# Kernel tuning notes

Measured on AMD Instinct MI355X. Metric: run time of the kernel, lower is better.

Reference implementation:

```python
import jax, jax.numpy as jnp
import numpy as np

H, DH = 16, 64  # heads, dim_head; inner = H*DH = 1024
EPS = 1e-5


def _ln(t, g, b):
    mu = jnp.mean(t, axis=-1, keepdims=True)
    var = jnp.var(t, axis=-1, keepdims=True)
    return (t - mu) * jax.lax.rsqrt(var + EPS) * g + b


def _split_heads(t):
    b, n, _ = t.shape
    return t.reshape(b, n, H, DH).transpose(0, 2, 1, 3)  # (b,h,n,dh)


def setup_inputs() -> dict:
    key = jax.random.key(0)
    ks = jax.random.split(key, 5)
    B, S, M, D = 16, 64, 4096, 1024  # S must equal DH (see source einsum quirk)
    return {
        "x": jax.random.normal(ks[0], (B, S, D), jnp.float32),
        "latents": jax.random.normal(ks[1], (B, M, D), jnp.float32),
        "ln_x_g": jnp.ones((D,), jnp.float32),
        "ln_x_b": jnp.zeros((D,), jnp.float32),
        "ln_l_g": jnp.ones((D,), jnp.float32),
        "ln_l_b": jnp.zeros((D,), jnp.float32),
        "Wq": jax.random.normal(ks[2], (D, H * DH), jnp.float32) * 0.02,
        "Wkv": jax.random.normal(ks[3], (D, 2 * H * DH), jnp.float32) * 0.02,
        "Wout": jax.random.normal(ks[4], (H * DH, D), jnp.float32) * 0.02,
    }


def reference(x, latents, ln_x_g, ln_x_b, ln_l_g, ln_l_b, Wq, Wkv, Wout):
    scale = DH ** -0.5
    xn = _ln(x, ln_x_g, ln_x_b)          # (B,S,D)
    ln = _ln(latents, ln_l_g, ln_l_b)    # (B,M,D)
    q = _split_heads(ln @ Wq) * scale    # (B,H,M,DH)
    k, v = map(_split_heads, jnp.split(xn @ Wkv, 2, axis=-1))  # (B,H,S,DH)
    sim = jnp.einsum('bhid,bhjd->bhij', q, k)                  # (B,H,M,S)
    sim = sim - jax.lax.stop_gradient(jnp.max(sim, axis=-1, keepdims=True))
    attn = jax.nn.softmax(sim, axis=-1)
    # Faithful to source: einsum('b h i d, b h j d -> b h i j', attn, v)
    # contracts attn's S dim with v's DH dim (requires S == DH); out = attn @ v^T.
    out = jnp.einsum('bhis,bhjs->bhij', attn, v)               # (B,H,M,S)
    b, _, m, _ = out.shape
    out = out.transpose(0, 2, 1, 3).reshape(b, m, H * DH)      # (B,M,inner)
    return out @ Wout                                          # (B,M,D)
```

## Files before the change

kernel.cpp:

```cpp
#include <hip/hip_runtime.h>
#include <stdint.h>

#define B_ 16
#define S_ 64
#define M_ 4096
#define D_ 1024
#define H_ 16
#define DH_ 64

typedef unsigned short ushort_t;
typedef __attribute__((ext_vector_type(8))) __bf16 bfrag;
typedef __attribute__((ext_vector_type(4))) float f32x4;

__device__ __forceinline__ ushort_t f2bf(float f) {
  union { float f; uint32_t u; } v; v.f = f;
  uint32_t r = v.u + 0x7fffu + ((v.u >> 16) & 1u);
  return (ushort_t)(r >> 16);
}

__device__ __forceinline__ void gload_lds16(const void* g, void* l) {
  __builtin_amdgcn_global_load_lds((const __attribute__((address_space(1))) void*)g,
                                   (__attribute__((address_space(3))) void*)l, 16, 0, 0);
}

__device__ __forceinline__ f32x4 mfma16x16x32(bfrag a, bfrag b, f32x4 c) {
  return __builtin_amdgcn_mfma_f32_16x16x32_bf16(a, b, c, 0, 0, 0);
}

__device__ __forceinline__ int fsw(int r) { return (((r >> 2) & 3) << 1) | (r & 1); }

__global__ __launch_bounds__(256) void ln_rows_kernel(
    const float* __restrict__ x, const float* __restrict__ g,
    const float* __restrict__ bta, ushort_t* __restrict__ out) {
  const int row = blockIdx.x;
  const int t = threadIdx.x;
  const float4* xr = (const float4*)(x + (size_t)row * D_);
  float4 v = xr[t];
  float s = v.x + v.y + v.z + v.w;
  float ss = v.x * v.x + v.y * v.y + v.z * v.z + v.w * v.w;
#pragma unroll
  for (int o = 32; o >= 1; o >>= 1) { s += __shfl_down(s, o); ss += __shfl_down(ss, o); }
  __shared__ float red[16];
  const int wid = t >> 6;
  if ((t & 63) == 0) { red[wid] = s; red[8 + wid] = ss; }
  __syncthreads();
  float tot = red[0] + red[1] + red[2] + red[3];
  float tot2 = red[8] + red[9] + red[10] + red[11];
  float mu = tot * (1.0f / D_);
  float var = tot2 * (1.0f / D_) - mu * mu;
  float rstd = rsqrtf(var + 1e-5f);
  float4 gg = ((const float4*)g)[t];
  float4 bb = ((const float4*)bta)[t];
  ushort_t ob[4];
  ob[0] = f2bf((v.x - mu) * rstd * gg.x + bb.x);
  ob[1] = f2bf((v.y - mu) * rstd * gg.y + bb.y);
  ob[2] = f2bf((v.z - mu) * rstd * gg.z + bb.z);
  ob[3] = f2bf((v.w - mu) * rstd * gg.w + bb.w);
  *(uint2*)(out + (size_t)row * D_ + t * 4) = *(const uint2*)ob;
}

__global__ void transpose_cast_kernel(const float* __restrict__ W, ushort_t* __restrict__ WT,
                                      int N, float scale) {
  __shared__ float tile[32][33];
  const int n0 = blockIdx.x * 32, k0 = blockIdx.y * 32;
  const int tx = threadIdx.x, ty = threadIdx.y;
#pragma unroll
  for (int i = ty; i < 32; i += 8)
    tile[i][tx] = W[(size_t)(k0 + i) * N + n0 + tx];
  __syncthreads();
#pragma unroll
  for (int i = ty; i < 32; i += 8)
    WT[(size_t)(n0 + i) * D_ + k0 + tx] = f2bf(tile[tx][i] * scale);
}

__global__ __launch_bounds__(256) void gemm_kv_kernel(
    const ushort_t* __restrict__ A, const ushort_t* __restrict__ Bt,
    ushort_t* __restrict__ kb, ushort_t* __restrict__ vb) {
  __shared__ __align__(16) ushort_t sA[128 * 32];
  __shared__ __align__(16) ushort_t sB[128 * 32];
  const int tid = threadIdx.x, wid = tid >> 6, lane = tid & 63;
  const size_t arow0 = (size_t)blockIdx.x * 128;
  const size_t brow0 = (size_t)blockIdx.y * 128;
  const int wr = (wid >> 1) * 64, wc = (wid & 1) * 64;
  const int srow = tid >> 2, scol = (tid & 3) * 8;
  const ushort_t* ga = A + (arow0 + srow) * (size_t)D_ + scol;
  const ushort_t* gb = Bt + (brow0 + srow) * (size_t)D_ + scol;
  const int frow = lane & 15, kslot = (lane >> 4) * 8;
  f32x4 acc[4][4] = {};
  for (int k0 = 0; k0 < D_; k0 += 32) {
    gload_lds16(ga, sA + wid * 512);
    gload_lds16(ga + 64 * (size_t)D_, sA + 2048 + wid * 512);
    gload_lds16(gb, sB + wid * 512);
    gload_lds16(gb + 64 * (size_t)D_, sB + 2048 + wid * 512);
    ga += 32; gb += 32;
    __syncthreads();
    bfrag af[4], bfv[4];
#pragma unroll
    for (int m = 0; m < 4; ++m)
      af[m] = *(const bfrag*)&sA[(wr + m * 16 + frow) * 32 + kslot];
#pragma unroll
    for (int n = 0; n < 4; ++n)
      bfv[n] = *(const bfrag*)&sB[(wc + n * 16 + frow) * 32 + kslot];
#pragma unroll
    for (int m = 0; m < 4; ++m)
#pragma unroll
      for (int n = 0; n < 4; ++n)
        acc[m][n] = mfma16x16x32(af[m], bfv[n], acc[m][n]);
    __syncthreads();
  }
  const int erow = (lane >> 4) * 4, ecol = lane & 15;
#pragma unroll
  for (int m = 0; m < 4; ++m)
#pragma unroll
    for (int n = 0; n < 4; ++n)
#pragma unroll
      for (int r = 0; r < 4; ++r) {
        size_t i = arow0 + wr + m * 16 + erow + r;
        int bb = (int)(i >> 6), s = (int)(i & 63);
        size_t n2 = brow0 + wc + n * 16 + ecol;
        ushort_t val = f2bf(acc[m][n][r]);
        ushort_t* dst = (n2 < 1024) ? kb : vb;
        size_t hh = (n2 & 1023) >> 6, d = n2 & 63;
        dst[(((size_t)bb * H_ + hh) * S_ + s) * DH_ + d] = val;
      }
}

template <int MODE>
__global__ __launch_bounds__(512, 2) void gemm256_kernel(
    const ushort_t* __restrict__ A, const ushort_t* __restrict__ Bt,
    const ushort_t* __restrict__ kbuf, const ushort_t* __restrict__ vbuf,
    void* __restrict__ Cout) {
  __shared__ __align__(16) ushort_t lds[65536];
  const int tid = threadIdx.x, wid = tid >> 6, lane = tid & 63;
  const int frow = lane & 15, klo = lane >> 4;
  const int wm = wid >> 2, wn = wid & 3;

  const int l = ((int)blockIdx.x & 7) * 128 + ((int)blockIdx.x >> 3);
  const int mblk = l >> 2, nblk = l & 3;
  const size_t arow0 = (size_t)mblk * 256;
  const size_t bcol0 = (size_t)nblk * 256;

  const int r0 = tid >> 2;
  const int gsrc = (tid & 3) ^ ((tid >> 3) & 3);
  const ushort_t* pA0 = A + (arow0 + r0) * (size_t)D_ + gsrc * 8;
  const ushort_t* pA1 = pA0 + (size_t)128 * D_;
  const ushort_t* pB0 = Bt + (bcol0 + r0) * (size_t)D_ + gsrc * 8;
  const ushort_t* pB1 = pB0 + (size_t)128 * D_;
  const int rasw = (klo ^ ((frow >> 1) & 3)) * 8;

#define STAGE_A(G)                                                            \
  do {                                                                        \
    const int s_ = (G) & 3;                                                   \
    const size_t ko_ = (size_t)((G) < 32 ? (G) : 31) * 32;                    \
    gload_lds16(pA0 + ko_, &lds[s_ * 8192 + wid * 512]);                      \
    gload_lds16(pA1 + ko_, &lds[s_ * 8192 + 4096 + wid * 512]);               \
  } while (0)
#define STAGE_B(G)                                                            \
  do {                                                                        \
    const int s_ = (G) & 3;                                                   \
    const size_t ko_ = (size_t)((G) < 32 ? (G) : 31) * 32;                    \
    gload_lds16(pB0 + ko_, &lds[32768 + s_ * 8192 + wid * 512]);              \
    gload_lds16(pB1 + ko_, &lds[32768 + s_ * 8192 + 4096 + wid * 512]);       \
  } while (0)

#define PHASE(KH, MH, STAGE_STMT, DO_WAIT)                                    \
  do {                                                                        \
    STAGE_STMT;                                                               \
    const ushort_t* As_ = &lds[((2 * t + (KH)) & 3) * 8192];                  \
    if ((MH) == 0) {                                                          \
      const ushort_t* Bs_ = &lds[32768 + ((2 * t + (KH)) & 3) * 8192];        \
      _Pragma("unroll") for (int nf = 0; nf < 4; ++nf)                        \
          bregs[nf] = *(const bfrag*)&Bs_[(wn * 64 + nf * 16 + frow) * 32 + rasw]; \
    }                                                                         \
    bfrag a_[4];                                                              \
    _Pragma("unroll") for (int mf = 0; mf < 4; ++mf)                          \
        a_[mf] = *(const bfrag*)&As_[(wm * 128 + (MH) * 64 + mf * 16 + frow) * 32 + rasw]; \
    if (DO_WAIT) asm volatile("s_waitcnt vmcnt(8)" ::: "memory");             \
    __builtin_amdgcn_s_barrier();                                             \
    asm volatile("s_waitcnt lgkmcnt(0)" ::: "memory");                        \
    __builtin_amdgcn_sched_barrier(0);                                        \
    __builtin_amdgcn_s_setprio(1);                                            \
    _Pragma("unroll") for (int mf = 0; mf < 4; ++mf)                          \
        _Pragma("unroll") for (int nf = 0; nf < 4; ++nf)                      \
            acc[(MH) * 4 + mf][nf] =                                          \
                mfma16x16x32(a_[mf], bregs[nf], acc[(MH) * 4 + mf][nf]);      \
    __builtin_amdgcn_s_setprio(0);                                            \
    __builtin_amdgcn_s_barrier();                                             \
  } while (0)

  STAGE_A(0); STAGE_B(0);
  STAGE_A(1); STAGE_B(1);
  STAGE_A(2); STAGE_B(2);
  asm volatile("s_waitcnt vmcnt(8)" ::: "memory");
  __builtin_amdgcn_s_barrier();

  f32x4 acc[8][4] = {};
  bfrag bregs[4];
  for (int t = 0; t < 16; ++t) {
    PHASE(0, 0, STAGE_A(2 * t + 3), 0);
    PHASE(0, 1, STAGE_B(2 * t + 3), 1);
    PHASE(1, 0, STAGE_A(2 * t + 4), 0);
    PHASE(1, 1, STAGE_B(2 * t + 4), 1);
  }
  asm volatile("s_waitcnt vmcnt(0)" ::: "memory");
  __builtin_amdgcn_s_barrier();
  __builtin_amdgcn_sched_barrier(0);
#undef PHASE
#undef STAGE_A
#undef STAGE_B

  if constexpr (MODE == 0) {
    float* C = (float*)Cout;
#pragma unroll
    for (int m = 0; m < 8; ++m)
#pragma unroll
      for (int n = 0; n < 4; ++n)
#pragma unroll
        for (int r = 0; r < 4; ++r)
          C[(arow0 + wm * 128 + m * 16 + klo * 4 + r) * 1024 + bcol0 + wn * 64 + n * 16 + frow] =
              acc[m][n][r];
  } else {
    ushort_t* W = &lds[wid * 4096];
    ushort_t* out1 = (ushort_t*)Cout;
    const int head = nblk * 4 + wn;
    const int bbatch = mblk >> 4;
    const size_t kvbase = ((size_t)bbatch * H_ + head) * (size_t)(S_ * DH_);
    bfrag kb[4][2], vb[4][2];
#pragma unroll
    for (int nf = 0; nf < 4; ++nf)
#pragma unroll
      for (int kk = 0; kk < 2; ++kk) {
        kb[nf][kk] = *(const bfrag*)&kbuf[kvbase + (nf * 16 + frow) * 64 + kk * 32 + klo * 8];
        vb[nf][kk] = *(const bfrag*)&vbuf[kvbase + (nf * 16 + frow) * 64 + kk * 32 + klo * 8];
      }
#pragma unroll
    for (int hh = 0; hh < 2; ++hh) {
#pragma unroll
      for (int m2 = 0; m2 < 4; ++m2)
#pragma unroll
        for (int r = 0; r < 4; ++r) {
          const int row = m2 * 16 + klo * 4 + r;
          const int fs = fsw(row);
#pragma unroll
          for (int n = 0; n < 4; ++n) {
            const int cc = n * 16 + frow;
            W[row * 64 + ((((cc >> 3) ^ fs) << 3) | (cc & 7))] = f2bf(acc[hh * 4 + m2][n][r]);
          }
        }
      f32x4 s[4][4] = {};
#pragma unroll
      for (int m2 = 0; m2 < 4; ++m2) {
        const int row = m2 * 16 + frow;
        const int fs = fsw(row);
#pragma unroll
        for (int kk = 0; kk < 2; ++kk) {
          bfrag qa = *(const bfrag*)&W[row * 64 + (((kk * 4 + klo) ^ fs) << 3)];
#pragma unroll
          for (int nf = 0; nf < 4; ++nf)
            s[m2][nf] = mfma16x16x32(qa, kb[nf][kk], s[m2][nf]);
        }
      }
#pragma unroll
      for (int m2 = 0; m2 < 4; ++m2)
#pragma unroll
        for (int r = 0; r < 4; ++r) {
          float a0 = s[m2][0][r], a1 = s[m2][1][r], a2 = s[m2][2][r], a3 = s[m2][3][r];
          float mx = fmaxf(fmaxf(a0, a1), fmaxf(a2, a3));
#pragma unroll
          for (int o = 1; o < 16; o <<= 1) mx = fmaxf(mx, __shfl_xor(mx, o));
          a0 = __expf(a0 - mx); a1 = __expf(a1 - mx);
          a2 = __expf(a2 - mx); a3 = __expf(a3 - mx);
          float sm = (a0 + a1) + (a2 + a3);
#pragma unroll
          for (int o = 1; o < 16; o <<= 1) sm += __shfl_xor(sm, o);
          const float inv = 1.0f / sm;
          s[m2][0][r] = a0 * inv; s[m2][1][r] = a1 * inv;
          s[m2][2][r] = a2 * inv; s[m2][3][r] = a3 * inv;
        }
#pragma unroll
      for (int m2 = 0; m2 < 4; ++m2)
#pragma unroll
        for (int r = 0; r < 4; ++r) {
          const int row = m2 * 16 + klo * 4 + r;
          const int fs = fsw(row);
#pragma unroll
          for (int n = 0; n < 4; ++n) {
            const int cc = n * 16 + frow;
            W[row * 64 + ((((cc >> 3) ^ fs) << 3) | (cc & 7))] = f2bf(s[m2][n][r]);
          }
        }
      f32x4 o[4][4] = {};
#pragma unroll
      for (int m2 = 0; m2 < 4; ++m2) {
        const int row = m2 * 16 + frow;
        const int fs = fsw(row);
#pragma unroll
        for (int kk = 0; kk < 2; ++kk) {
          bfrag pa = *(const bfrag*)&W[row * 64 + (((kk * 4 + klo) ^ fs) << 3)];
#pragma unroll
          for (int nf = 0; nf < 4; ++nf)
            o[m2][nf] = mfma16x16x32(pa, vb[nf][kk], o[m2][nf]);
        }
      }
#pragma unroll
      for (int m2 = 0; m2 < 4; ++m2)
#pragma unroll
        for (int r = 0; r < 4; ++r) {
          const int row = m2 * 16 + klo * 4 + r;
          const int fs = fsw(row);
#pragma unroll
          for (int n = 0; n < 4; ++n) {
            const int cc = n * 16 + frow;
            W[row * 64 + ((((cc >> 3) ^ fs) << 3) | (cc & 7))] = f2bf(o[m2][n][r]);
          }
        }
      const size_t grow0 = arow0 + wm * 128 + hh * 64;
#pragma unroll
      for (int it = 0; it < 8; ++it) {
        const int idx = it * 64 + lane;
        const int rr = idx >> 3, gs = idx & 7;
        const int gcol = (gs ^ fsw(rr)) << 3;
        *(uint4*)&out1[(grow0 + rr) * 1024 + head * 64 + gcol] =
            *(const uint4*)&W[rr * 64 + gs * 8];
      }
    }
  }
}

extern "C" void kernel_launch(void* const* d_in, const int* in_sizes, int n_in,
                              void* d_out, int out_size, void* d_ws, size_t ws_size,
                              hipStream_t stream) {
  const float* x = (const float*)d_in[0];
  const float* lat = (const float*)d_in[1];
  const float* lxg = (const float*)d_in[2];
  const float* lxb = (const float*)d_in[3];
  const float* llg = (const float*)d_in[4];
  const float* llb = (const float*)d_in[5];
  const float* Wq = (const float*)d_in[6];
  const float* Wkv = (const float*)d_in[7];
  const float* Wout = (const float*)d_in[8];
  float* out = (float*)d_out;
  char* ws = (char*)d_ws;

  ushort_t* xn = (ushort_t*)(ws);
  ushort_t* wqT = (ushort_t*)(ws + (2ull << 20));
  ushort_t* wkvT = (ushort_t*)(ws + (4ull << 20));
  ushort_t* woT = (ushort_t*)(ws + (8ull << 20));
  ushort_t* kbuf = (ushort_t*)(ws + (10ull << 20));
  ushort_t* vbuf = (ushort_t*)(ws + (12ull << 20));
  ushort_t* out1 = (ushort_t*)(ws + (14ull << 20));
  ushort_t* lnl = (ushort_t*)d_out;

  dim3 tb(32, 8);
  transpose_cast_kernel<<<dim3(1024 / 32, 32), tb, 0, stream>>>(Wq, wqT, 1024, 0.125f);
  transpose_cast_kernel<<<dim3(2048 / 32, 32), tb, 0, stream>>>(Wkv, wkvT, 2048, 1.0f);
  transpose_cast_kernel<<<dim3(1024 / 32, 32), tb, 0, stream>>>(Wout, woT, 1024, 1.0f);
  ln_rows_kernel<<<B_ * S_, 256, 0, stream>>>(x, lxg, lxb, xn);
  ln_rows_kernel<<<B_ * M_, 256, 0, stream>>>(lat, llg, llb, lnl);
  gemm_kv_kernel<<<dim3(8, 16), 256, 0, stream>>>(xn, wkvT, kbuf, vbuf);
  gemm256_kernel<1><<<1024, 512, 0, stream>>>(lnl, wqT, kbuf, vbuf, out1);
  gemm256_kernel<0><<<1024, 512, 0, stream>>>(out1, woT, nullptr, nullptr, out);
}
```

Baseline: 472.7 us.

## Software-pipeline LDS fragment loads with MFMA via double-buffered register fragments

Restructures the GEMM main loop so the LDS reads of the next A/B fragments are issued between MFMA instructions of the current half-tile, using current/next register buffers. Loop runs per k-step with two barriers instead of four phases, and global-to-LDS staging is reordered with adjusted vmcnt waits. This aims to hide LDS read latency behind matrix-core work, at the cost of extra VGPRs and more delicate buffer-reuse synchronisation.

```diff
diff --git a/kernel.cpp b/kernel.cpp
--- a/kernel.cpp
+++ b/kernel.cpp
@@ -163,49 +163,67 @@
     gload_lds16(pB1 + ko_, &lds[32768 + s_ * 8192 + 4096 + wid * 512]);       \
   } while (0)
 
-#define PHASE(KH, MH, STAGE_STMT, DO_WAIT)                                    \
-  do {                                                                        \
-    STAGE_STMT;                                                               \
-    const ushort_t* As_ = &lds[((2 * t + (KH)) & 3) * 8192];                  \
-    if ((MH) == 0) {                                                          \
-      const ushort_t* Bs_ = &lds[32768 + ((2 * t + (KH)) & 3) * 8192];        \
-      _Pragma("unroll") for (int nf = 0; nf < 4; ++nf)                        \
-          bregs[nf] = *(const bfrag*)&Bs_[(wn * 64 + nf * 16 + frow) * 32 + rasw]; \
-    }                                                                         \
-    bfrag a_[4];                                                              \
-    _Pragma("unroll") for (int mf = 0; mf < 4; ++mf)                          \
-        a_[mf] = *(const bfrag*)&As_[(wm * 128 + (MH) * 64 + mf * 16 + frow) * 32 + rasw]; \
-    if (DO_WAIT) asm volatile("s_waitcnt vmcnt(8)" ::: "memory");             \
-    __builtin_amdgcn_s_barrier();                                             \
-    asm volatile("s_waitcnt lgkmcnt(0)" ::: "memory");                        \
-    __builtin_amdgcn_sched_barrier(0);                                        \
-    __builtin_amdgcn_s_setprio(1);                                            \
-    _Pragma("unroll") for (int mf = 0; mf < 4; ++mf)                          \
-        _Pragma("unroll") for (int nf = 0; nf < 4; ++nf)                      \
-            acc[(MH) * 4 + mf][nf] =                                          \
-                mfma16x16x32(a_[mf], bregs[nf], acc[(MH) * 4 + mf][nf]);      \
-    __builtin_amdgcn_s_setprio(0);                                            \
-    __builtin_amdgcn_s_barrier();                                             \
-  } while (0)
-
   STAGE_A(0); STAGE_B(0);
   STAGE_A(1); STAGE_B(1);
   STAGE_A(2); STAGE_B(2);
   asm volatile("s_waitcnt vmcnt(8)" ::: "memory");
   __builtin_amdgcn_s_barrier();
+  bfrag aC[4], aN[4], bC[4], bN[4];
+  {
+    const ushort_t* As = &lds[0];
+    const ushort_t* Bs = &lds[32768];
+#pragma unroll
+    for (int mf = 0; mf < 4; ++mf)
+      aC[mf] = *(const bfrag*)&As[(wm * 128 + mf * 16 + frow) * 32 + rasw];
+#pragma unroll
+    for (int nf = 0; nf < 4; ++nf)
+      bC[nf] = *(const bfrag*)&Bs[(wn * 64 + nf * 16 + frow) * 32 + rasw];
+  }
 
   f32x4 acc[8][4] = {};
-  bfrag bregs[4];
-  for (int t = 0; t < 16; ++t) {
-    PHASE(0, 0, STAGE_A(2 * t + 3), 0);
-    PHASE(0, 1, STAGE_B(2 * t + 3), 1);
-    PHASE(1, 0, STAGE_A(2 * t + 4), 0);
-    PHASE(1, 1, STAGE_B(2 * t + 4), 1);
+  for (int g = 0; g < 32; ++g) {
+    __builtin_amdgcn_s_barrier();
+    asm volatile("s_waitcnt lgkmcnt(0)" ::: "memory");
+    __builtin_amdgcn_sched_barrier(0);
+    __builtin_amdgcn_s_setprio(1);
+    {
+      const ushort_t* As = &lds[(g & 3) * 8192];
+#pragma unroll
+      for (int mf = 0; mf < 4; ++mf) {
+#pragma unroll
+        for (int nf = 0; nf < 4; ++nf)
+          acc[mf][nf] = mfma16x16x32(aC[mf], bC[nf], acc[mf][nf]);
+        aN[mf] = *(const bfrag*)&As[(wm * 128 + 64 + mf * 16 + frow) * 32 + rasw];
+      }
+    }
+    __builtin_amdgcn_s_setprio(0);
+    STAGE_A(g + 3);
+    asm volatile("s_waitcnt vmcnt(6)" ::: "memory");
+    __builtin_amdgcn_s_barrier();
+    asm volatile("s_waitcnt lgkmcnt(0)" ::: "memory");
+    __builtin_amdgcn_sched_barrier(0);
+    __builtin_amdgcn_s_setprio(1);
+    {
+      const int gn = (g + 1 < 32) ? g + 1 : 31;
+      const ushort_t* As2 = &lds[(gn & 3) * 8192];
+      const ushort_t* Bs2 = &lds[32768 + (gn & 3) * 8192];
+#pragma unroll
+      for (int mf = 0; mf < 4; ++mf) {
+#pragma unroll
+        for (int nf = 0; nf < 4; ++nf)
+          acc[4 + mf][nf] = mfma16x16x32(aN[mf], bC[nf], acc[4 + mf][nf]);
+        aC[mf] = *(const bfrag*)&As2[(wm * 128 + mf * 16 + frow) * 32 + rasw];
+        bN[mf] = *(const bfrag*)&Bs2[(wn * 64 + mf * 16 + frow) * 32 + rasw];
+      }
+    }
+    __builtin_amdgcn_s_setprio(0);
+    STAGE_B(g + 3);
+#pragma unroll
+    for (int nf = 0; nf < 4; ++nf) bC[nf] = bN[nf];
   }
   asm volatile("s_waitcnt vmcnt(0)" ::: "memory");
   __builtin_amdgcn_s_barrier();
   __builtin_amdgcn_sched_barrier(0);
-#undef PHASE
 #undef STAGE_A
 #undef STAGE_B
 
```

Result: no change. 465.4 us (-1.5%).
